# Optimization experiments

Hardware: AMD Instinct MI355X
Metric: run time of the kernel (lower is better)

## Reference

```python
import jax, jax.numpy as jnp
import numpy as np

B, L = 256, 32768

def _avg_pool1d(x, k, p):
    # count_include_pad=True avg pool via prefix sums: O(L) instead of O(L*k)
    xp = jnp.pad(x, ((0, 0), (0, 0), (p, p)))
    cs = jnp.cumsum(xp, axis=-1)
    cs = jnp.pad(cs, ((0, 0), (0, 0), (1, 0)))  # leading zero for window diff
    return (cs[..., k:] - cs[..., :-k]) / k

def setup_inputs() -> dict:
    key = jax.random.key(0)
    x = jax.random.normal(key, (B, L), dtype=jnp.float32)
    return {"x": x}

def reference(x):
    x = x[:, None, :]  # [B, 1, L]
    # log(max(1, 1+x)) and log(max(1, 1-x)): cat-with-ones + max == clamp at 1
    a = jnp.log(jnp.maximum(1.0, 1.0 + x))
    b = jnp.log(jnp.maximum(1.0, 1.0 - x))
    a0 = _avg_pool1d(a, 3, 1)
    a5 = _avg_pool1d(a, 199, 99)
    b0 = _avg_pool1d(b, 3, 1)
    b5 = _avg_pool1d(b, 199, 99)
    return jnp.concatenate([a0 - a5, a0, b0 - b5, b0], axis=1)  # [B, 4, L]
```

## Files before the change

kernel.cpp:

```cpp
#include <hip/hip_runtime.h>

#define B_DIM 256
#define L_DIM 32768
#define CHUNK 2048
#define HALO  100
#define NTOT  (CHUNK + 2*HALO)
#define NG    (NTOT/4)
#define T     256
#define EPT   9
#define NCH   2
#define NR    3

typedef float fx4 __attribute__((ext_vector_type(4)));

__device__ __forceinline__ void issue_loads(const float* __restrict__ xr, int chunk0,
                                            int tid, fx4 p[NR]) {
    #pragma unroll
    for (int r = 0; r < NR; ++r) {
        const int g = tid + r * T;
        if (g < NG) {
            const int c = chunk0 - HALO + 4 * g;
            if (c >= 0 && c + 3 < L_DIM) {
                p[r] = *reinterpret_cast<const fx4*>(xr + c);
            } else {
                p[r].x = (c + 0 >= 0 && c + 0 < L_DIM) ? xr[c + 0] : 0.0f;
                p[r].y = (c + 1 >= 0 && c + 1 < L_DIM) ? xr[c + 1] : 0.0f;
                p[r].z = (c + 2 >= 0 && c + 2 < L_DIM) ? xr[c + 2] : 0.0f;
                p[r].w = (c + 3 >= 0 && c + 3 < L_DIM) ? xr[c + 3] : 0.0f;
            }
        }
    }
}

__global__ __launch_bounds__(T) void pool_feat_kernel(const float* __restrict__ x,
                                                      float* __restrict__ out) {
    const int row  = blockIdx.y;
    const int base = blockIdx.x * (CHUNK * NCH);
    const int tid  = threadIdx.x;

    __shared__ __align__(16) float sA[NTOT];
    __shared__ __align__(16) float sB[NTOT];
    __shared__ float waveA[4];
    __shared__ float waveB[4];

    const float* xr = x + (size_t)row * L_DIM;

    fx4 pc[NR], pn[NR];
    issue_loads(xr, base, tid, pc);

    for (int k = 0; k < NCH; ++k) {
        const int chunk0 = base + k * CHUNK;

        #pragma unroll
        for (int r = 0; r < NR; ++r) {
            const int g = tid + r * T;
            if (g < NG) *reinterpret_cast<fx4*>(&sA[4 * g]) = pc[r];
        }
        if (k + 1 < NCH) issue_loads(xr, chunk0 + CHUNK, tid, pn);
        __syncthreads();

        const int s0 = tid * EPT;
        const int s1 = min(NTOT, s0 + EPT);
        float runA = 0.0f, runB = 0.0f;
        for (int j = s0; j < s1; ++j) {
            const float v = sA[j];
            const float t = __logf(1.0f + fabsf(v));
            const float u = copysignf(t, v);
            runA += fmaxf(u, 0.0f);
            runB += fmaxf(-u, 0.0f);
            sA[j] = u;
        }

        float vA = runA, vB = runB;
        const int lane = tid & 63;
        const int wid  = tid >> 6;
        #pragma unroll
        for (int d = 1; d < 64; d <<= 1) {
            float uA = __shfl_up(vA, d);
            float uB = __shfl_up(vB, d);
            if (lane >= d) { vA += uA; vB += uB; }
        }
        if (lane == 63) { waveA[wid] = vA; waveB[wid] = vB; }
        __syncthreads();
        float offA = vA - runA;
        float offB = vB - runB;
        #pragma unroll
        for (int w = 0; w < 3; ++w) {
            if (w < wid) { offA += waveA[w]; offB += waveB[w]; }
        }

        float accA = offA, accB = offB;
        for (int j = s0; j < s1; ++j) {
            const float u = sA[j];
            accA += fmaxf(u, 0.0f);
            accB += fmaxf(-u, 0.0f);
            sA[j] = accA;
            sB[j] = accB;
        }
        __syncthreads();

        const float inv3   = 1.0f / 3.0f;
        const float inv199 = 1.0f / 199.0f;
        float* ob = out + (size_t)row * 4u * L_DIM + chunk0;
        #pragma unroll
        for (int it = 0; it < CHUNK / (4 * T); ++it) {
            const int i0 = 4 * (tid + it * T);
            fx4 r0, r1, r2, r3;
            #pragma unroll
            for (int arr = 0; arr < 2; ++arr) {
                const float* s = arr ? sB : sA;
                const fx4 L0 = *reinterpret_cast<const fx4*>(s + i0);
                const fx4 L1 = *reinterpret_cast<const fx4*>(s + i0 + 96);
                const fx4 L2 = *reinterpret_cast<const fx4*>(s + i0 + 100);
                const fx4 L3 = *reinterpret_cast<const fx4*>(s + i0 + 104);
                const fx4 L4 = *reinterpret_cast<const fx4*>(s + i0 + 196);
                const fx4 L5 = *reinterpret_cast<const fx4*>(s + i0 + 200);
                const float csI[4]   = {L0.x, L0.y, L0.z, L0.w};
                const float cs98[4]  = {L1.z, L1.w, L2.x, L2.y};
                const float cs101[4] = {L2.y, L2.z, L2.w, L3.x};
                const float cs199[4] = {L4.w, L5.x, L5.y, L5.z};
                fx4& rs = arr ? r3 : r1;
                fx4& rd = arr ? r2 : r0;
                #pragma unroll
                for (int u = 0; u < 4; ++u) {
                    const float p0 = (cs101[u] - cs98[u]) * inv3;
                    const float p5 = (cs199[u] - csI[u]) * inv199;
                    rs[u] = p0;
                    rd[u] = p0 - p5;
                }
            }
            *reinterpret_cast<fx4*>(ob + 0 * (size_t)L_DIM + i0) = r0;
            *reinterpret_cast<fx4*>(ob + 1 * (size_t)L_DIM + i0) = r1;
            *reinterpret_cast<fx4*>(ob + 2 * (size_t)L_DIM + i0) = r2;
            *reinterpret_cast<fx4*>(ob + 3 * (size_t)L_DIM + i0) = r3;
        }

        if (k + 1 < NCH) {
            __syncthreads();
            #pragma unroll
            for (int r = 0; r < NR; ++r) pc[r] = pn[r];
        }
    }
}

extern "C" void kernel_launch(void* const* d_in, const int* in_sizes, int n_in,
                              void* d_out, int out_size, void* d_ws, size_t ws_size,
                              hipStream_t stream) {
    const float* x = (const float*)d_in[0];
    float* out = (float*)d_out;
    dim3 grid(L_DIM / (CHUNK * NCH), B_DIM);
    pool_feat_kernel<<<grid, dim3(T), 0, stream>>>(x, out);
}
```

Measured before the change: 31.10 us.

## Load each thread's contiguous scan segment into registers, skip LDS staging

Each thread now loads its own contiguous 12-element segment straight from global memory into registers. The log transform and local prefix sums run in registers, and the scanned values go to LDS with vector stores. This drops the LDS write/read round trip and one barrier per chunk. The trade-off is that only 188 of 256 threads do scan work, and the global loads become less coalesced because each thread reads a strided 48-byte span. The next-chunk prefetch is also issued earlier.

```diff
diff --git a/kernel.cpp b/kernel.cpp
--- a/kernel.cpp
+++ b/kernel.cpp
@@ -5,28 +5,34 @@
 #define CHUNK 2048
 #define HALO  100
 #define NTOT  (CHUNK + 2*HALO)
-#define NG    (NTOT/4)
+#define NTOTP 2256
 #define T     256
-#define EPT   9
+#define EPT   12
+#define NSEG  188
 #define NCH   2
-#define NR    3
 
 typedef float fx4 __attribute__((ext_vector_type(4)));
 
 __device__ __forceinline__ void issue_loads(const float* __restrict__ xr, int chunk0,
-                                            int tid, fx4 p[NR]) {
-    #pragma unroll
-    for (int r = 0; r < NR; ++r) {
-        const int g = tid + r * T;
-        if (g < NG) {
-            const int c = chunk0 - HALO + 4 * g;
-            if (c >= 0 && c + 3 < L_DIM) {
-                p[r] = *reinterpret_cast<const fx4*>(xr + c);
-            } else {
-                p[r].x = (c + 0 >= 0 && c + 0 < L_DIM) ? xr[c + 0] : 0.0f;
-                p[r].y = (c + 1 >= 0 && c + 1 < L_DIM) ? xr[c + 1] : 0.0f;
-                p[r].z = (c + 2 >= 0 && c + 2 < L_DIM) ? xr[c + 2] : 0.0f;
-                p[r].w = (c + 3 >= 0 && c + 3 < L_DIM) ? xr[c + 3] : 0.0f;
+                                            int tid, fx4 p[3]) {
+    if (tid >= NSEG) {
+        p[0] = (fx4)0.0f; p[1] = (fx4)0.0f; p[2] = (fx4)0.0f;
+        return;
+    }
+    const int gbase = chunk0 - HALO + EPT * tid;
+    if (tid < NSEG - 1 && gbase >= 0 && gbase + EPT <= L_DIM) {
+        p[0] = *reinterpret_cast<const fx4*>(xr + gbase);
+        p[1] = *reinterpret_cast<const fx4*>(xr + gbase + 4);
+        p[2] = *reinterpret_cast<const fx4*>(xr + gbase + 8);
+    } else {
+        const int idx0 = EPT * tid;
+        #pragma unroll
+        for (int r = 0; r < 3; ++r) {
+            #pragma unroll
+            for (int c = 0; c < 4; ++c) {
+                const int idx = idx0 + 4 * r + c;
+                const int col = gbase + 4 * r + c;
+                p[r][c] = (idx < NTOT && col >= 0 && col < L_DIM) ? xr[col] : 0.0f;
             }
         }
     }
@@ -38,37 +44,34 @@
     const int base = blockIdx.x * (CHUNK * NCH);
     const int tid  = threadIdx.x;
 
-    __shared__ __align__(16) float sA[NTOT];
-    __shared__ __align__(16) float sB[NTOT];
+    __shared__ __align__(16) float sA[NTOTP];
+    __shared__ __align__(16) float sB[NTOTP];
     __shared__ float waveA[4];
     __shared__ float waveB[4];
 
     const float* xr = x + (size_t)row * L_DIM;
 
-    fx4 pc[NR], pn[NR];
+    fx4 pc[3], pn[3];
     issue_loads(xr, base, tid, pc);
 
     for (int k = 0; k < NCH; ++k) {
         const int chunk0 = base + k * CHUNK;
 
+        if (k + 1 < NCH) issue_loads(xr, chunk0 + CHUNK, tid, pn);
+
+        float u[EPT];
+        float runA = 0.0f, runB = 0.0f;
         #pragma unroll
-        for (int r = 0; r < NR; ++r) {
-            const int g = tid + r * T;
-            if (g < NG) *reinterpret_cast<fx4*>(&sA[4 * g]) = pc[r];
-        }
-        if (k + 1 < NCH) issue_loads(xr, chunk0 + CHUNK, tid, pn);
-        __syncthreads();
-
-        const int s0 = tid * EPT;
-        const int s1 = min(NTOT, s0 + EPT);
-        float runA = 0.0f, runB = 0.0f;
-        for (int j = s0; j < s1; ++j) {
-            const float v = sA[j];
-            const float t = __logf(1.0f + fabsf(v));
-            const float u = copysignf(t, v);
-            runA += fmaxf(u, 0.0f);
-            runB += fmaxf(-u, 0.0f);
-            sA[j] = u;
+        for (int r = 0; r < 3; ++r) {
+            #pragma unroll
+            for (int c = 0; c < 4; ++c) {
+                const float v  = pc[r][c];
+                const float t  = __logf(1.0f + fabsf(v));
+                const float uu = copysignf(t, v);
+                runA += fmaxf(uu, 0.0f);
+                runB += fmaxf(-uu, 0.0f);
+                u[4 * r + c] = uu;
+            }
         }
 
         float vA = runA, vB = runB;
@@ -89,13 +92,23 @@
             if (w < wid) { offA += waveA[w]; offB += waveB[w]; }
         }
 
-        float accA = offA, accB = offB;
-        for (int j = s0; j < s1; ++j) {
-            const float u = sA[j];
-            accA += fmaxf(u, 0.0f);
-            accB += fmaxf(-u, 0.0f);
-            sA[j] = accA;
-            sB[j] = accB;
+        if (tid < NSEG) {
+            float accA = offA, accB = offB;
+            const int s0 = EPT * tid;
+            #pragma unroll
+            for (int r = 0; r < 3; ++r) {
+                fx4 wa, wb;
+                #pragma unroll
+                for (int c = 0; c < 4; ++c) {
+                    const float uu = u[4 * r + c];
+                    accA += fmaxf(uu, 0.0f);
+                    accB += fmaxf(-uu, 0.0f);
+                    wa[c] = accA;
+                    wb[c] = accB;
+                }
+                *reinterpret_cast<fx4*>(&sA[s0 + 4 * r]) = wa;
+                *reinterpret_cast<fx4*>(&sB[s0 + 4 * r]) = wb;
+            }
         }
         __syncthreads();
 
@@ -122,11 +135,11 @@
                 fx4& rs = arr ? r3 : r1;
                 fx4& rd = arr ? r2 : r0;
                 #pragma unroll
-                for (int u = 0; u < 4; ++u) {
-                    const float p0 = (cs101[u] - cs98[u]) * inv3;
-                    const float p5 = (cs199[u] - csI[u]) * inv199;
-                    rs[u] = p0;
-                    rd[u] = p0 - p5;
+                for (int q = 0; q < 4; ++q) {
+                    const float p0 = (cs101[q] - cs98[q]) * inv3;
+                    const float p5 = (cs199[q] - csI[q]) * inv199;
+                    rs[q] = p0;
+                    rd[q] = p0 - p5;
                 }
             }
             *reinterpret_cast<fx4*>(ob + 0 * (size_t)L_DIM + i0) = r0;
@@ -138,7 +151,7 @@
         if (k + 1 < NCH) {
             __syncthreads();
             #pragma unroll
-            for (int r = 0; r < NR; ++r) pc[r] = pn[r];
+            for (int r = 0; r < 3; ++r) pc[r] = pn[r];
         }
     }
 }
```

Result: slower. 32.09 us (+3.2%).
